# Optimization experiments

Hardware: AMD Instinct MI355X
Metric: run time of the kernel (lower is better)

The kernel has to match this reference:

```python
import jax, jax.numpy as jnp
import numpy as np

B, NQ, NK, DQ, DK, DV, H = 4, 512, 512, 512, 512, 512, 128
NEG_INF = -1e20


def setup_inputs() -> dict:
    key = jax.random.key(0)
    ks = jax.random.split(key, 7)
    Q = jax.random.normal(ks[0], (B, NQ, DQ), dtype=jnp.float32)
    K = jax.random.normal(ks[1], (B, NK, DK), dtype=jnp.float32)
    V = jax.random.normal(ks[2], (B, NK, DV), dtype=jnp.float32)
    # learned params (LazyLinear, bias=False): y = x @ W with W[in, out]
    Wq = jax.random.normal(ks[3], (DQ, H), dtype=jnp.float32) / np.sqrt(DQ)
    Wk = jax.random.normal(ks[4], (DK, H), dtype=jnp.float32) / np.sqrt(DK)
    wv = jax.random.normal(ks[5], (H,), dtype=jnp.float32) / np.sqrt(H)
    valid_lens = jax.random.randint(ks[6], (B,), 1, NK + 1).astype(jnp.int64)
    return {"Q": Q, "K": K, "V": V, "Wq": Wq, "Wk": Wk, "wv": wv,
            "valid_lens": valid_lens}


def reference(Q, K, V, Wq, Wk, wv, valid_lens):
    # Project queries and keys to shared hidden size H
    Qp = Q @ Wq                      # (B, NQ, H)
    Kp = K @ Wk                      # (B, NK, H)
    # Additive (Bahdanau) broadcast: (B, NQ, NK, H)
    S = jnp.tanh(Qp[:, :, None, :] + Kp[:, None, :, :])
    # Linear score to scalar: (B, NQ, NK)
    scores = jnp.einsum('bqkh,h->bqk', S, wv)
    # Mask positions k >= valid_lens[b] (1-D valid_lens broadcast over queries)
    kv_idx = jnp.arange(scores.shape[-1])[None, None, :]
    mask = kv_idx < valid_lens[:, None, None]
    scores = jnp.where(mask, scores, NEG_INF)
    W = jax.nn.softmax(scores, axis=-1)  # dropout rate 0.0 -> identity
    return jnp.einsum('bqk,bkv->bqv', W, V)
```

## Files before the change

kernel.cpp:

```cpp
#include <hip/hip_runtime.h>

#define B_   4
#define NQ_  512
#define NK_  512
#define D_   512
#define H_   128

typedef __attribute__((ext_vector_type(8))) short short8;
typedef __attribute__((ext_vector_type(4))) float f32x4;

__device__ __forceinline__ float fexp2(float x) { return __builtin_amdgcn_exp2f(x); }
__device__ __forceinline__ float frcp(float x)  { return __builtin_amdgcn_rcpf(x); }
__device__ __forceinline__ unsigned short f2bf(float f) {
    unsigned int u = __builtin_bit_cast(unsigned int, f);
    u += 0x7FFFu + ((u >> 16) & 1u);
    return (unsigned short)(u >> 16);
}


#define WS_EQK   0
#define WS_WP    524288
#define WS_WBF   524544
#define WS_VT    1048832

__global__ __launch_bounds__(256) void prep2_kernel(
    const float* __restrict__ Q, const float* __restrict__ K,
    const float* __restrict__ Wq, const float* __restrict__ Wk,
    const float* __restrict__ V, const float* __restrict__ wv,
    float* __restrict__ Eqk, float* __restrict__ wp,
    unsigned short* __restrict__ Vt)
{
    __shared__ __align__(16) float smem[64 * 36 + 64 * 68];
    const int t = threadIdx.x;
    const float C2 = 2.88539008177792681472f;

    if (blockIdx.x == 0 && t < 64) {
        const float2 w2 = reinterpret_cast<const float2*>(wv)[t];
        const float wn0 = -2.0f * w2.x;
        const float wn1 = -2.0f * w2.y;
        reinterpret_cast<float4*>(wp)[t] =
            make_float4(wn0, wn1, wn0 + wn1, 0.0f);
    }

    if (blockIdx.x < 256) {
        const int rt = blockIdx.x >> 1;
        const int ct = blockIdx.x & 1;
        const int r0 = rt * 32;
        const bool isQ = r0 < 2048;
        const float* __restrict__ X = isQ ? Q : K;
        const float* __restrict__ W = isQ ? Wq : Wk;
        const int xr0 = isQ ? r0 : r0 - 2048;
        const int c0  = ct * 64;

        float (*At)[36] = (float(*)[36])smem;
        float (*Wl)[68] = (float(*)[68])(smem + 64 * 36);

        const int cg = t & 15;
        const int rg = t >> 4;
        float acc[2][4] = {};

        for (int kc = 0; kc < 8; ++kc) {
            const int k0 = kc * 64;
            if (kc) __syncthreads();
            #pragma unroll
            for (int p = 0; p < 2; ++p) {
                const int idx = p * 256 + t;
                const int row = idx >> 4;
                const int kq  = (idx & 15) * 4;
                const float4 v = *reinterpret_cast<const float4*>(
                    X + (size_t)(xr0 + row) * D_ + k0 + kq);
                At[kq + 0][row] = v.x; At[kq + 1][row] = v.y;
                At[kq + 2][row] = v.z; At[kq + 3][row] = v.w;
            }
            #pragma unroll
            for (int p = 0; p < 4; ++p) {
                const int idx = p * 256 + t;
                const int kr  = idx >> 4;
                const int c4  = (idx & 15) * 4;
                *reinterpret_cast<float4*>(&Wl[kr][c4]) =
                    *reinterpret_cast<const float4*>(
                        W + (size_t)(k0 + kr) * H_ + c0 + c4);
            }
            __syncthreads();

            #pragma unroll 8
            for (int k = 0; k < 64; ++k) {
                const float a0 = At[k][rg * 2];
                const float a1 = At[k][rg * 2 + 1];
                const float4 b4 = *reinterpret_cast<const float4*>(&Wl[k][cg * 4]);
                const float bb[4] = {b4.x, b4.y, b4.z, b4.w};
                #pragma unroll
                for (int c = 0; c < 4; ++c) {
                    acc[0][c] = fmaf(a0, bb[c], acc[0][c]);
                    acc[1][c] = fmaf(a1, bb[c], acc[1][c]);
                }
            }
        }

        #pragma unroll
        for (int r = 0; r < 2; ++r) {
            float4 o;
            o.x = fexp2(C2 * acc[r][0]); o.y = fexp2(C2 * acc[r][1]);
            o.z = fexp2(C2 * acc[r][2]); o.w = fexp2(C2 * acc[r][3]);
            *reinterpret_cast<float4*>(
                Eqk + (size_t)(r0 + rg * 2 + r) * H_ + c0 + cg * 4) = o;
        }
    } else {
        const int id = blockIdx.x - 256;
        const int kt = id & 7, dt = (id >> 3) & 7, b = id >> 6;
        float (*Vl)[69] = (float(*)[69])smem;

        #pragma unroll
        for (int p = 0; p < 4; ++p) {
            const int idx = p * 256 + t;
            const int r  = idx >> 4;
            const int c4 = (idx & 15) * 4;
            const float4 v = *reinterpret_cast<const float4*>(
                V + ((size_t)b * NK_ + kt * 64 + r) * D_ + dt * 64 + c4);
            Vl[r][c4 + 0] = v.x; Vl[r][c4 + 1] = v.y;
            Vl[r][c4 + 2] = v.z; Vl[r][c4 + 3] = v.w;
        }
        __syncthreads();

        #pragma unroll
        for (int p = 0; p < 4; ++p) {
            const int idx = p * 256 + t;
            const int d  = idx >> 4;
            const int k4 = (idx & 15) * 4;
            ushort4 o;
            o.x = f2bf(Vl[k4 + 0][d]); o.y = f2bf(Vl[k4 + 1][d]);
            o.z = f2bf(Vl[k4 + 2][d]); o.w = f2bf(Vl[k4 + 3][d]);
            *reinterpret_cast<ushort4*>(
                Vt + ((size_t)b * D_ + dt * 64 + d) * NK_ + kt * 64 + k4) = o;
        }
    }
}

__global__ __launch_bounds__(512, 4) void score_softmax_kernel(
    const float* __restrict__ Eqk, const float* __restrict__ wp,
    const int* __restrict__ valid_lens, unsigned short* __restrict__ Wbf)
{
    const int rb   = blockIdx.x;
    const int t    = threadIdx.x;
    const int w    = __builtin_amdgcn_readfirstlane(t >> 6);
    const int lane = t & 63;
    const int rloc = w >> 1;
    const int half = w & 1;
    const int row  = rb * 4 + rloc;
    const int b    = row >> 9;

    __shared__ __align__(16) float4 Ks[2 * 64 * 33];
    __shared__ float redM[4][2], redS[4][2];

    const float4* __restrict__ Q4 =
        reinterpret_cast<const float4*>(Eqk + (size_t)row * H_);
    const float4* __restrict__ wp4 = reinterpret_cast<const float4*>(wp);
    const float4* __restrict__ Kp4 =
        reinterpret_cast<const float4*>(Eqk + (size_t)(2048 + b * NK_) * H_);

    float vals[4];

    for (int c = 0; c < 4; ++c) {
        if (c) __syncthreads();
        #pragma unroll
        for (int p = 0; p < 8; ++p) {
            const int idx = p * 512 + t;
            const int hh  = idx >> 11;
            const int r   = (idx >> 5) & 63;
            const int h4  = idx & 31;
            Ks[(hh * 64 + r) * 33 + h4] =
                Kp4[(size_t)(hh * 256 + c * 64 + r) * 32 + h4];
        }
        __syncthreads();

        float s = 0.0f;
        #pragma unroll 4
        for (int g = 0; g < 32; ++g) {
            const float4 kv = Ks[(half * 64 + lane) * 33 + g];
            const float4 qa = Q4[g];
            const float4 wa = wp4[2 * g];
            const float4 wb = wp4[2 * g + 1];
            const float e0 = qa.x * kv.x;
            const float e1 = qa.y * kv.y;
            const float e2 = qa.z * kv.z;
            const float e3 = qa.w * kv.w;
            const float D01 = 1.0f + fmaf(e0, e1, e0 + e1);
            const float D23 = 1.0f + fmaf(e2, e3, e2 + e3);
            const float n01 = fmaf(wa.y, e0, fmaf(wa.x, e1, wa.z));
            const float n23 = fmaf(wb.y, e2, fmaf(wb.x, e3, wb.z));
            const float N   = fmaf(n23, D01, n01 * D23);
            s = fmaf(N, frcp(D01 * D23), s);
        }
        vals[c] = s;
    }

    const int vl = valid_lens[b];
    const float L2E = 1.44269504088896340736f;
    float m = -1e30f;
    #pragma unroll
    for (int c = 0; c < 4; ++c) {
        const int k = half * 256 + c * 64 + lane;
        vals[c] = (k < vl) ? vals[c] : -1e30f;
        m = fmaxf(m, vals[c]);
    }
    #pragma unroll
    for (int off = 32; off >= 1; off >>= 1)
        m = fmaxf(m, __shfl_xor(m, off, 64));
    float sum = 0.0f;
    #pragma unroll
    for (int c = 0; c < 4; ++c)
        sum += fexp2((vals[c] - m) * L2E);
    #pragma unroll
    for (int off = 32; off >= 1; off >>= 1)
        sum += __shfl_xor(sum, off, 64);

    if (lane == 0) { redM[rloc][half] = m; redS[rloc][half] = sum; }
    __syncthreads();

    const float m0 = redM[rloc][0], m1 = redM[rloc][1];
    const float s0 = redS[rloc][0], s1 = redS[rloc][1];
    const float M  = fmaxf(m0, m1);
    const float S  = fmaf(s0, fexp2((m0 - M) * L2E),
                          s1 * fexp2((m1 - M) * L2E));
    const float inv = frcp(S);

    unsigned short* __restrict__ dst = Wbf + (size_t)row * NK_ + half * 256;
    #pragma unroll
    for (int c = 0; c < 4; ++c)
        dst[c * 64 + lane] = f2bf(fexp2((vals[c] - M) * L2E) * inv);
}

__global__ __launch_bounds__(256) void av_gemm_kernel(
    const unsigned short* __restrict__ Wbf, const unsigned short* __restrict__ Vt,
    float* __restrict__ O)
{
    const int c0 = blockIdx.x * 64;
    const int r0 = blockIdx.y * 64;
    const int b  = blockIdx.z;
    const int t  = threadIdx.x;
    const int wave = __builtin_amdgcn_readfirstlane(t >> 6);
    const int lane = t & 63;
    const int m    = lane & 15;
    const int quad = lane >> 4;

    __shared__ unsigned short Al [64][136];
    __shared__ unsigned short Btl[64][136];

    f32x4 acc0 = {0.f,0.f,0.f,0.f}, acc1 = {0.f,0.f,0.f,0.f};
    f32x4 acc2 = {0.f,0.f,0.f,0.f}, acc3 = {0.f,0.f,0.f,0.f};

    for (int kc = 0; kc < 4; ++kc) {
        if (kc) __syncthreads();
        #pragma unroll
        for (int p = 0; p < 4; ++p) {
            const int idx = p * 256 + t;
            const int rl = idx >> 4;
            const int k8 = (idx & 15) * 8;
            *reinterpret_cast<uint4*>(&Al[rl][k8]) =
                *reinterpret_cast<const uint4*>(
                    Wbf + ((size_t)b * NQ_ + r0 + rl) * NK_ + kc * 128 + k8);
            *reinterpret_cast<uint4*>(&Btl[rl][k8]) =
                *reinterpret_cast<const uint4*>(
                    Vt + ((size_t)b * D_ + c0 + rl) * NK_ + kc * 128 + k8);
        }
        __syncthreads();

        #pragma unroll
        for (int sub = 0; sub < 4; ++sub) {
            const int kcol = sub * 32 + quad * 8;
            const short8 a = *reinterpret_cast<const short8*>(&Al[wave * 16 + m][kcol]);
            const short8 b0 = *reinterpret_cast<const short8*>(&Btl[ 0 + m][kcol]);
            const short8 b1 = *reinterpret_cast<const short8*>(&Btl[16 + m][kcol]);
            const short8 b2 = *reinterpret_cast<const short8*>(&Btl[32 + m][kcol]);
            const short8 b3 = *reinterpret_cast<const short8*>(&Btl[48 + m][kcol]);
            acc0 = __builtin_amdgcn_mfma_f32_16x16x32_bf16(a, b0, acc0, 0, 0, 0);
            acc1 = __builtin_amdgcn_mfma_f32_16x16x32_bf16(a, b1, acc1, 0, 0, 0);
            acc2 = __builtin_amdgcn_mfma_f32_16x16x32_bf16(a, b2, acc2, 0, 0, 0);
            acc3 = __builtin_amdgcn_mfma_f32_16x16x32_bf16(a, b3, acc3, 0, 0, 0);
        }
    }

    const size_t rowbase = (size_t)b * NQ_ + r0 + wave * 16 + quad * 4;
    #pragma unroll
    for (int i = 0; i < 4; ++i) {
        float* __restrict__ orow = O + (rowbase + i) * D_ + c0 + m;
        orow[ 0] = acc0[i];
        orow[16] = acc1[i];
        orow[32] = acc2[i];
        orow[48] = acc3[i];
    }
}

extern "C" void kernel_launch(void* const* d_in, const int* in_sizes, int n_in,
                              void* d_out, int out_size, void* d_ws, size_t ws_size,
                              hipStream_t stream) {
    (void)in_sizes; (void)n_in; (void)out_size; (void)ws_size;

    const float* Q   = (const float*)d_in[0];
    const float* K   = (const float*)d_in[1];
    const float* V   = (const float*)d_in[2];
    const float* Wq  = (const float*)d_in[3];
    const float* Wk  = (const float*)d_in[4];
    const float* wv  = (const float*)d_in[5];
    const int*   vl  = (const int*)d_in[6];
    float* out = (float*)d_out;

    float* ws  = (float*)d_ws;
    float* Eqk = ws + WS_EQK;
    float* wp  = ws + WS_WP;
    unsigned short* Wbf = (unsigned short*)(ws + WS_WBF);
    unsigned short* Vt  = (unsigned short*)(ws + WS_VT);

    prep2_kernel<<<dim3(512), 256, 0, stream>>>(Q, K, Wq, Wk, V, wv, Eqk, wp, Vt);
    score_softmax_kernel<<<dim3(512), 512, 0, stream>>>(Eqk, wp, vl, Wbf);
    av_gemm_kernel<<<dim3(8, 8, 4), 256, 0, stream>>>(Wbf, Vt, out);
}
```

Before: 118.5 us.

## Move Q/K projection to split-bf16 MFMA in a dedicated kernel

Replaces the scalar FP32 FMA projection GEMM with a separate kernel that uses bf16 MFMA instructions. Inputs and weights are split into hi/lo bf16 parts, and three MFMAs (hi*hi, lo*hi, hi*lo) recover near-FP32 accuracy. The prep kernel now only transposes V and pre-splits and transposes the weights. The aim is to cut the ALU-bound projection time, at the cost of an extra kernel launch and extra workspace traffic.

```diff
diff --git a/kernel.cpp b/kernel.cpp
--- a/kernel.cpp
+++ b/kernel.cpp
@@ -7,6 +7,7 @@
 #define H_   128
 
 typedef __attribute__((ext_vector_type(8))) short short8;
+typedef __attribute__((ext_vector_type(8))) unsigned short ushort8;
 typedef __attribute__((ext_vector_type(4))) float f32x4;
 
 __device__ __forceinline__ float fexp2(float x) { return __builtin_amdgcn_exp2f(x); }
@@ -16,97 +17,29 @@
     u += 0x7FFFu + ((u >> 16) & 1u);
     return (unsigned short)(u >> 16);
 }
+__device__ __forceinline__ float bf2f(unsigned short h) {
+    return __builtin_bit_cast(float, (unsigned int)h << 16);
+}
 
 
 #define WS_EQK   0
 #define WS_WP    524288
 #define WS_WBF   524544
 #define WS_VT    1048832
-
-__global__ __launch_bounds__(256) void prep2_kernel(
-    const float* __restrict__ Q, const float* __restrict__ K,
-    const float* __restrict__ Wq, const float* __restrict__ Wk,
-    const float* __restrict__ V, const float* __restrict__ wv,
-    float* __restrict__ Eqk, float* __restrict__ wp,
-    unsigned short* __restrict__ Vt)
+#define WS_WTHI  1573120
+#define WS_WTLO  1638656
+
+__global__ __launch_bounds__(256) void prep_kernel(
+    const float* __restrict__ V, const float* __restrict__ Wq,
+    const float* __restrict__ Wk, const float* __restrict__ wv,
+    float* __restrict__ wp, unsigned short* __restrict__ Vt,
+    unsigned short* __restrict__ WThi, unsigned short* __restrict__ WTlo)
 {
-    __shared__ __align__(16) float smem[64 * 36 + 64 * 68];
+    __shared__ __align__(16) float smem[64 * 69];
     const int t = threadIdx.x;
-    const float C2 = 2.88539008177792681472f;
-
-    if (blockIdx.x == 0 && t < 64) {
-        const float2 w2 = reinterpret_cast<const float2*>(wv)[t];
-        const float wn0 = -2.0f * w2.x;
-        const float wn1 = -2.0f * w2.y;
-        reinterpret_cast<float4*>(wp)[t] =
-            make_float4(wn0, wn1, wn0 + wn1, 0.0f);
-    }
 
     if (blockIdx.x < 256) {
-        const int rt = blockIdx.x >> 1;
-        const int ct = blockIdx.x & 1;
-        const int r0 = rt * 32;
-        const bool isQ = r0 < 2048;
-        const float* __restrict__ X = isQ ? Q : K;
-        const float* __restrict__ W = isQ ? Wq : Wk;
-        const int xr0 = isQ ? r0 : r0 - 2048;
-        const int c0  = ct * 64;
-
-        float (*At)[36] = (float(*)[36])smem;
-        float (*Wl)[68] = (float(*)[68])(smem + 64 * 36);
-
-        const int cg = t & 15;
-        const int rg = t >> 4;
-        float acc[2][4] = {};
-
-        for (int kc = 0; kc < 8; ++kc) {
-            const int k0 = kc * 64;
-            if (kc) __syncthreads();
-            #pragma unroll
-            for (int p = 0; p < 2; ++p) {
-                const int idx = p * 256 + t;
-                const int row = idx >> 4;
-                const int kq  = (idx & 15) * 4;
-                const float4 v = *reinterpret_cast<const float4*>(
-                    X + (size_t)(xr0 + row) * D_ + k0 + kq);
-                At[kq + 0][row] = v.x; At[kq + 1][row] = v.y;
-                At[kq + 2][row] = v.z; At[kq + 3][row] = v.w;
-            }
-            #pragma unroll
-            for (int p = 0; p < 4; ++p) {
-                const int idx = p * 256 + t;
-                const int kr  = idx >> 4;
-                const int c4  = (idx & 15) * 4;
-                *reinterpret_cast<float4*>(&Wl[kr][c4]) =
-                    *reinterpret_cast<const float4*>(
-                        W + (size_t)(k0 + kr) * H_ + c0 + c4);
-            }
-            __syncthreads();
-
-            #pragma unroll 8
-            for (int k = 0; k < 64; ++k) {
-                const float a0 = At[k][rg * 2];
-                const float a1 = At[k][rg * 2 + 1];
-                const float4 b4 = *reinterpret_cast<const float4*>(&Wl[k][cg * 4]);
-                const float bb[4] = {b4.x, b4.y, b4.z, b4.w};
-                #pragma unroll
-                for (int c = 0; c < 4; ++c) {
-                    acc[0][c] = fmaf(a0, bb[c], acc[0][c]);
-                    acc[1][c] = fmaf(a1, bb[c], acc[1][c]);
-                }
-            }
-        }
-
-        #pragma unroll
-        for (int r = 0; r < 2; ++r) {
-            float4 o;
-            o.x = fexp2(C2 * acc[r][0]); o.y = fexp2(C2 * acc[r][1]);
-            o.z = fexp2(C2 * acc[r][2]); o.w = fexp2(C2 * acc[r][3]);
-            *reinterpret_cast<float4*>(
-                Eqk + (size_t)(r0 + rg * 2 + r) * H_ + c0 + cg * 4) = o;
-        }
-    } else {
-        const int id = blockIdx.x - 256;
+        const int id = blockIdx.x;
         const int kt = id & 7, dt = (id >> 3) & 7, b = id >> 6;
         float (*Vl)[69] = (float(*)[69])smem;
 
@@ -133,6 +66,121 @@
             *reinterpret_cast<ushort4*>(
                 Vt + ((size_t)b * D_ + dt * 64 + d) * NK_ + kt * 64 + k4) = o;
         }
+    } else {
+        if (blockIdx.x == 256 && t < 64) {
+            const float2 w2 = reinterpret_cast<const float2*>(wv)[t];
+            const float wn0 = -2.0f * w2.x;
+            const float wn1 = -2.0f * w2.y;
+            reinterpret_cast<float4*>(wp)[t] =
+                make_float4(wn0, wn1, wn0 + wn1, 0.0f);
+        }
+        const int wid  = blockIdx.x - 256;
+        const int mat  = wid >> 4;
+        const int tile = wid & 15;
+        const int kt   = tile >> 1;
+        const int ct   = tile & 1;
+        const float* __restrict__ Wm = mat ? Wk : Wq;
+        float (*Wl)[69] = (float(*)[69])smem;
+
+        #pragma unroll
+        for (int p = 0; p < 4; ++p) {
+            const int idx = p * 256 + t;
+            const int r  = idx >> 4;
+            const int c4 = (idx & 15) * 4;
+            const float4 v = *reinterpret_cast<const float4*>(
+                Wm + (size_t)(kt * 64 + r) * H_ + ct * 64 + c4);
+            Wl[r][c4 + 0] = v.x; Wl[r][c4 + 1] = v.y;
+            Wl[r][c4 + 2] = v.z; Wl[r][c4 + 3] = v.w;
+        }
+        __syncthreads();
+
+        const int c  = t >> 2;
+        const int kq = (t & 3) * 16;
+        ushort8 ph0, pl0, ph1, pl1;
+        #pragma unroll
+        for (int j = 0; j < 8; ++j) {
+            const float x = Wl[kq + j][c];
+            const unsigned short h = f2bf(x);
+            ph0[j] = h; pl0[j] = f2bf(x - bf2f(h));
+        }
+        #pragma unroll
+        for (int j = 0; j < 8; ++j) {
+            const float x = Wl[kq + 8 + j][c];
+            const unsigned short h = f2bf(x);
+            ph1[j] = h; pl1[j] = f2bf(x - bf2f(h));
+        }
+        const size_t off =
+            ((size_t)(mat * H_ + ct * 64 + c)) * 512 + kt * 64 + kq;
+        *reinterpret_cast<ushort8*>(WThi + off)     = ph0;
+        *reinterpret_cast<ushort8*>(WThi + off + 8) = ph1;
+        *reinterpret_cast<ushort8*>(WTlo + off)     = pl0;
+        *reinterpret_cast<ushort8*>(WTlo + off + 8) = pl1;
+    }
+}
+
+__global__ __launch_bounds__(512, 2) void proj_kernel(
+    const float* __restrict__ Q, const float* __restrict__ K,
+    const unsigned short* __restrict__ WThi,
+    const unsigned short* __restrict__ WTlo,
+    float* __restrict__ Eqk)
+{
+    __shared__ __align__(16) unsigned short Ahi[16][520];
+    __shared__ __align__(16) unsigned short Alo[16][520];
+    const int t  = threadIdx.x;
+    const int r0 = blockIdx.x * 16;
+    const bool isQ = r0 < 2048;
+    const float* __restrict__ X = isQ ? Q : K;
+    const int xr0    = isQ ? r0 : r0 - 2048;
+    const int matoff = isQ ? 0 : (H_ * 512);
+
+    #pragma unroll
+    for (int p = 0; p < 4; ++p) {
+        const int idx = p * 512 + t;
+        const int row = idx >> 7;
+        const int kq  = (idx & 127) * 4;
+        const float4 v = *reinterpret_cast<const float4*>(
+            X + (size_t)(xr0 + row) * D_ + kq);
+        ushort4 h, l;
+        h.x = f2bf(v.x); l.x = f2bf(v.x - bf2f(h.x));
+        h.y = f2bf(v.y); l.y = f2bf(v.y - bf2f(h.y));
+        h.z = f2bf(v.z); l.z = f2bf(v.z - bf2f(h.z));
+        h.w = f2bf(v.w); l.w = f2bf(v.w - bf2f(h.w));
+        *reinterpret_cast<ushort4*>(&Ahi[row][kq]) = h;
+        *reinterpret_cast<ushort4*>(&Alo[row][kq]) = l;
+    }
+    __syncthreads();
+
+    const int wave = __builtin_amdgcn_readfirstlane(t >> 6);
+    const int lane = t & 63;
+    const int m    = lane & 15;
+    const int quad = lane >> 4;
+
+    const unsigned short* __restrict__ Bh =
+        WThi + matoff + ((size_t)(wave * 16 + m)) * 512 + quad * 8;
+    const unsigned short* __restrict__ Bl =
+        WTlo + matoff + ((size_t)(wave * 16 + m)) * 512 + quad * 8;
+
+    f32x4 accA = {0.f, 0.f, 0.f, 0.f};
+    f32x4 accB = {0.f, 0.f, 0.f, 0.f};
+    #pragma unroll
+    for (int ksg = 0; ksg < 16; ++ksg) {
+        const int kk = ksg * 32;
+        const short8 bh = *reinterpret_cast<const short8*>(Bh + kk);
+        const short8 bl = *reinterpret_cast<const short8*>(Bl + kk);
+        const short8 ah = *reinterpret_cast<const short8*>(&Ahi[m][kk + quad * 8]);
+        const short8 al = *reinterpret_cast<const short8*>(&Alo[m][kk + quad * 8]);
+        f32x4& acc = (ksg & 1) ? accB : accA;
+        acc = __builtin_amdgcn_mfma_f32_16x16x32_bf16(ah, bh, acc, 0, 0, 0);
+        acc = __builtin_amdgcn_mfma_f32_16x16x32_bf16(al, bh, acc, 0, 0, 0);
+        acc = __builtin_amdgcn_mfma_f32_16x16x32_bf16(ah, bl, acc, 0, 0, 0);
+    }
+
+    const float C2 = 2.88539008177792681472f;
+    const int col = wave * 16 + m;
+    #pragma unroll
+    for (int i = 0; i < 4; ++i) {
+        Eqk[(size_t)(r0 + quad * 4 + i) * H_ + col] =
+            fexp2(C2 * (accA[i] + accB[i]));
     }
 }
 
@@ -308,10 +356,13 @@
     float* ws  = (float*)d_ws;
     float* Eqk = ws + WS_EQK;
     float* wp  = ws + WS_WP;
-    unsigned short* Wbf = (unsigned short*)(ws + WS_WBF);
-    unsigned short* Vt  = (unsigned short*)(ws + WS_VT);
-
-    prep2_kernel<<<dim3(512), 256, 0, stream>>>(Q, K, Wq, Wk, V, wv, Eqk, wp, Vt);
+    unsigned short* Wbf  = (unsigned short*)(ws + WS_WBF);
+    unsigned short* Vt   = (unsigned short*)(ws + WS_VT);
+    unsigned short* WThi = (unsigned short*)(ws + WS_WTHI);
+    unsigned short* WTlo = (unsigned short*)(ws + WS_WTLO);
+
+    prep_kernel<<<dim3(288), 256, 0, stream>>>(V, Wq, Wk, wv, wp, Vt, WThi, WTlo);
+    proj_kernel<<<dim3(256), 512, 0, stream>>>(Q, K, WThi, WTlo, Eqk);
     score_softmax_kernel<<<dim3(512), 512, 0, stream>>>(Eqk, wp, vl, Wbf);
     av_gemm_kernel<<<dim3(8, 8, 4), 256, 0, stream>>>(Wbf, Vt, out);
 }
```

Measured after the change: 115.1 us. -2.8%, faster.
